# Performance work log

Measured on AMD Instinct MI355X. Metric: run time of the kernel, lower is better.

Reference implementation:

```python
import jax, jax.numpy as jnp
import numpy as np

S = 100000   # unique_source_num
T = 20000    # unique_target_num
N = S + T    # total nodes (sources first, then targets)
E = 1000000  # edges
SRC_DIM, EMB_DIM, TGT_DIM = 256, 128, 128


def setup_inputs() -> dict:
    key = jax.random.key(0)
    ks = jax.random.split(key, 6)
    source_feat = jax.random.normal(ks[0], (N, SRC_DIM), dtype=jnp.float32)
    src_idx = jax.random.randint(ks[1], (E,), 0, S)            # edge sources in [0, S)
    dst_idx = jax.random.randint(ks[2], (E,), 0, T)            # edge targets, target-local in [0, T)
    range_list = jax.random.randint(ks[3], (T, 2), 0, S)       # unused by the math (passed through in torch)
    # x_norm divides features; keep it bounded away from 0 like real row norms
    x_norm = jax.random.uniform(ks[4], (N,), dtype=jnp.float32, minval=0.5, maxval=1.5)
    k_e, k_w = jax.random.split(ks[5])
    embed = jax.random.normal(k_e, (SRC_DIM, EMB_DIM), dtype=jnp.float32)          # Param, std=1 init
    weight = jax.random.normal(k_w, (EMB_DIM, TGT_DIM), dtype=jnp.float32) / np.sqrt(EMB_DIM)  # is_after_relu std=1/sqrt(in)
    return {"source_feat": source_feat, "src_idx": src_idx, "dst_idx": dst_idx,
            "range_list": range_list, "x_norm": x_norm, "embed": embed, "weight": weight}


def reference(source_feat, src_idx, dst_idx, range_list, x_norm, embed, weight):
    # x = (source_feat @ embed) / x_norm[:, None]   -> [N, EMB_DIM]
    x = jnp.matmul(source_feat, embed) / x_norm[:, None]
    # message + scatter-mean aggregation onto targets (sources receive no edges,
    # so aggregating directly over the T targets == aggr_out[S:] in the torch code)
    msgs = x[src_idx]                                           # [E, EMB_DIM] gather
    summed = jax.ops.segment_sum(msgs, dst_idx, num_segments=T) # [T, EMB_DIM]
    cnt = jax.ops.segment_sum(jnp.ones((E,), dtype=x.dtype), dst_idx, num_segments=T)
    aggr = summed / jnp.maximum(cnt, 1.0)[:, None]              # mean; zero-degree -> 0
    out = jnp.matmul(aggr, weight)                              # [T, TGT_DIM]
    return out
```

## Files before the change

### kernel.cpp

```cpp
#include <hip/hip_runtime.h>
#include <cstdint>
#include <cstddef>

#define S_NUM 100000
#define T_NUM 20000
#define E_NUM 1000000

#define NB   1250
#define GT   16
#define CAP  1280
#define CH   4096
#define KB2  245
#define KB1  1563

typedef __bf16 bf16x8 __attribute__((ext_vector_type(8)));
typedef float f32x4 __attribute__((ext_vector_type(4)));

__device__ __forceinline__ unsigned short f2bf(float f) {
  unsigned int u = __float_as_uint(f);
  u += 0x7fffu + ((u >> 16) & 1u);
  return (unsigned short)(u >> 16);
}
__device__ __forceinline__ unsigned int f2bf2(float lo, float hi) {
  return (unsigned int)f2bf(lo) | ((unsigned int)f2bf(hi) << 16);
}
__device__ __forceinline__ float bflo(unsigned int v) { return __uint_as_float(v << 16); }
__device__ __forceinline__ float bfhi(unsigned int v) { return __uint_as_float(v & 0xffff0000u); }

__launch_bounds__(256)
__global__ void k0_prep(const float* __restrict__ embed, const float* __restrict__ weight,
                        int* __restrict__ gcursor, unsigned short* __restrict__ embedT,
                        unsigned short* __restrict__ weightT) {
  const int idx = blockIdx.x * 256 + threadIdx.x;
  if (idx < 2048) gcursor[idx] = 0;
  {
    const int col = idx & 127;
    const int k = idx >> 7;
    embedT[(size_t)col * 256 + k] = f2bf(embed[(size_t)k * 128 + col]);
  }
  if (idx < 16384) {
    const int n = idx & 127;
    const int k = idx >> 7;
    weightT[(size_t)n * 128 + k] = f2bf(weight[(size_t)k * 128 + n]);
  }
}

__launch_bounds__(512)
__global__ void k12_fused(const float* __restrict__ sf, const float* __restrict__ xn,
                          const unsigned short* __restrict__ embedT, unsigned short* __restrict__ xb,
                          const int* __restrict__ src_idx, const int* __restrict__ dst_idx,
                          int* __restrict__ gcursor, unsigned int* __restrict__ ebuf) {
  __shared__ __align__(16) unsigned char smem[64 * 296 * 2];
  const int tid = threadIdx.x;

  if (blockIdx.x < KB2) {
    int* bcnt  = (int*)smem;
    int* gbase = (int*)(smem + 5120);
    const int e0 = blockIdx.x * CH;
    const int e1 = (e0 + CH < E_NUM) ? (e0 + CH) : E_NUM;
    for (int i = tid; i < NB; i += 512) bcnt[i] = 0;
    __syncthreads();
    for (int e = e0 + tid; e < e1; e += 512)
      atomicAdd(&bcnt[dst_idx[e] >> 4], 1);
    __syncthreads();
    for (int i = tid; i < NB; i += 512) {
      const int cnt = bcnt[i];
      gbase[i] = (cnt > 0) ? atomicAdd(&gcursor[i], cnt) : 0;
      bcnt[i] = 0;
    }
    __syncthreads();
    for (int e = e0 + tid; e < e1; e += 512) {
      const int d = dst_idx[e];
      const int s = src_idx[e];
      const int b = d >> 4;
      const int r = atomicAdd(&bcnt[b], 1);
      const int pos = gbase[b] + r;
      if (pos < CAP)
        ebuf[(size_t)b * CAP + pos] = ((unsigned int)(d & 15) << 17) | (unsigned int)s;
    }
    return;
  }

  unsigned short (*lA)[296] = (unsigned short (*)[296])smem;
  unsigned short (*lC)[136] = (unsigned short (*)[136])smem;
  const int wave = tid >> 6;
  const int lane = tid & 63;
  const int quad = lane >> 4;
  const int l15 = lane & 15;
  const int row0 = (blockIdx.x - KB2) * 64;
  const int col0 = wave * 16;

  const unsigned short* ebT = embedT + (size_t)(col0 + l15) * 256;
  bf16x8 fb[8];
#pragma unroll
  for (int kc = 0; kc < 8; ++kc)
    fb[kc] = *(const bf16x8*)(ebT + kc * 32 + quad * 8);

#pragma unroll
  for (int i = 0; i < 4; ++i) {
    const int idx = i * 512 + tid;
    const int row = idx >> 5;
    const int seg = idx & 31;
    const float4* g = (const float4*)(sf + (size_t)(row0 + row) * 256 + seg * 8);
    const float4 v0 = g[0];
    const float4 v1 = g[1];
    uint4 pk;
    pk.x = f2bf2(v0.x, v0.y);
    pk.y = f2bf2(v0.z, v0.w);
    pk.z = f2bf2(v1.x, v1.y);
    pk.w = f2bf2(v1.z, v1.w);
    *(uint4*)&lA[row][seg * 8] = pk;
  }
  __syncthreads();

  f32x4 acc[4];
#pragma unroll
  for (int i = 0; i < 4; ++i) acc[i] = (f32x4){0.f, 0.f, 0.f, 0.f};

#pragma unroll
  for (int kc = 0; kc < 8; ++kc)
#pragma unroll
    for (int rt = 0; rt < 4; ++rt) {
      bf16x8 fa = *(const bf16x8*)&lA[rt * 16 + l15][kc * 32 + quad * 8];
      acc[rt] = __builtin_amdgcn_mfma_f32_16x16x32_bf16(fa, fb[kc], acc[rt], 0, 0, 0);
    }
  __syncthreads();

#pragma unroll
  for (int rt = 0; rt < 4; ++rt) {
#pragma unroll
    for (int reg = 0; reg < 4; ++reg) {
      const int row = rt * 16 + quad * 4 + reg;
      const float inv = __builtin_amdgcn_rcpf(xn[row0 + row]);
      lC[row][col0 + l15] = f2bf(acc[rt][reg] * inv);
    }
  }
  __syncthreads();

#pragma unroll
  for (int p = 0; p < 2; ++p) {
    const int i = p * 512 + tid;
    const int row = i >> 4;
    const int seg = i & 15;
    const int gr = row0 + row;
    if (gr < S_NUM)
      *(uint4*)(xb + (size_t)gr * 128 + seg * 8) = *(const uint4*)&lC[row][seg * 8];
  }
}

__launch_bounds__(512)
__global__ void k3_fused(const int* __restrict__ gcursor, const unsigned int* __restrict__ ebuf,
                         const unsigned short* __restrict__ xb,
                         const unsigned short* __restrict__ weightT,
                         float* __restrict__ out) {
  __shared__ unsigned int sls[CAP];
  __shared__ int hist[GT], scn[GT], cur[GT];
  __shared__ unsigned int Pu[GT][68];
  const int b = blockIdx.x;
  const int tid = threadIdx.x;
  const int wave = tid >> 6, lane = tid & 63;
  const int quad = lane >> 4, l15 = lane & 15;

  int n = gcursor[b];
  if (n > CAP) n = CAP;
  const unsigned int* eb = ebuf + (size_t)b * CAP;

  if (tid < GT) hist[tid] = 0;
  __syncthreads();
  for (int i = tid; i < n; i += 512) atomicAdd(&hist[eb[i] >> 17], 1);
  __syncthreads();
  if (tid == 0) {
    int run = 0;
#pragma unroll
    for (int i = 0; i < GT; ++i) { scn[i] = run; run += hist[i]; }
  }
  __syncthreads();
  if (tid < GT) cur[tid] = scn[tid];
  __syncthreads();
  for (int i = tid; i < n; i += 512) {
    const unsigned int e = eb[i];
    const int r = atomicAdd(&cur[e >> 17], 1);
    sls[r] = e & 0x1FFFFu;
  }
  __syncthreads();

  const int h = lane >> 5;
  const int cq = lane & 31;
#pragma unroll
  for (int rep = 0; rep < 2; ++rep) {
    const int tl = wave * 2 + rep;
    const int beg = scn[tl];
    const int c = hist[tl];
    float t0 = 0.f, t1 = 0.f, t2 = 0.f, t3 = 0.f;
    int e = 0;
    for (; e + 16 <= c; e += 16) {
      int s[8];
#pragma unroll
      for (int j = 0; j < 8; ++j) s[j] = (int)sls[beg + e + 2 * j + h];
      uint2 v[8];
#pragma unroll
      for (int j = 0; j < 8; ++j)
        v[j] = *(const uint2*)(xb + (size_t)s[j] * 128 + 4 * cq);
#pragma unroll
      for (int j = 0; j < 8; ++j) {
        t0 += bflo(v[j].x); t1 += bfhi(v[j].x);
        t2 += bflo(v[j].y); t3 += bfhi(v[j].y);
      }
    }
    for (; e + 2 <= c; e += 2) {
      const int s0 = (int)sls[beg + e + h];
      const uint2 v0 = *(const uint2*)(xb + (size_t)s0 * 128 + 4 * cq);
      t0 += bflo(v0.x); t1 += bfhi(v0.x);
      t2 += bflo(v0.y); t3 += bfhi(v0.y);
    }
    if ((c & 1) && h == 0) {
      const int s0 = (int)sls[beg + c - 1];
      const uint2 v0 = *(const uint2*)(xb + (size_t)s0 * 128 + 4 * cq);
      t0 += bflo(v0.x); t1 += bfhi(v0.x);
      t2 += bflo(v0.y); t3 += bfhi(v0.y);
    }
    t0 += __shfl_xor(t0, 32, 64);
    t1 += __shfl_xor(t1, 32, 64);
    t2 += __shfl_xor(t2, 32, 64);
    t3 += __shfl_xor(t3, 32, 64);
    const float inv = (c > 0) ? __builtin_amdgcn_rcpf((float)c) : 0.f;
    const unsigned int pk = h ? f2bf2(t2 * inv, t3 * inv) : f2bf2(t0 * inv, t1 * inv);
    Pu[tl][2 * cq + h] = pk;
  }
  __syncthreads();

  const int ncol = wave * 16 + l15;
  const unsigned short* wT = weightT + (size_t)ncol * 128;
  bf16x8 wb[4];
#pragma unroll
  for (int kc = 0; kc < 4; ++kc)
    wb[kc] = *(const bf16x8*)(wT + kc * 32 + quad * 8);
  f32x4 o0 = (f32x4){0.f, 0.f, 0.f, 0.f};
#pragma unroll
  for (int kc = 0; kc < 4; ++kc) {
    bf16x8 p0 = *(const bf16x8*)((const unsigned short*)&Pu[l15][0] + kc * 32 + quad * 8);
    o0 = __builtin_amdgcn_mfma_f32_16x16x32_bf16(p0, wb[kc], o0, 0, 0, 0);
  }
#pragma unroll
  for (int reg = 0; reg < 4; ++reg)
    out[((size_t)b * GT + quad * 4 + reg) * 128 + ncol] = o0[reg];
}

extern "C" void kernel_launch(void* const* d_in, const int* in_sizes, int n_in,
                              void* d_out, int out_size, void* d_ws, size_t ws_size,
                              hipStream_t stream) {
  const float* sf      = (const float*)d_in[0];
  const int*   src_idx = (const int*)d_in[1];
  const int*   dst_idx = (const int*)d_in[2];
  const float* xn      = (const float*)d_in[4];
  const float* embed   = (const float*)d_in[5];
  const float* weight  = (const float*)d_in[6];
  float* out = (float*)d_out;

  char* w = (char*)d_ws;
  unsigned short* xb      = (unsigned short*)(w);
  int* gcursor            = (int*)(w + 25600000);
  unsigned int* ebuf      = (unsigned int*)(w + 25608192);
  unsigned short* embedT  = (unsigned short*)(w + 32008192);
  unsigned short* weightT = (unsigned short*)(w + 32073728);

  k0_prep<<<128, 256, 0, stream>>>(embed, weight, gcursor, embedT, weightT);
  k12_fused<<<KB2 + KB1, 512, 0, stream>>>(sf, xn, embedT, xb, src_idx, dst_idx, gcursor, ebuf);
  k3_fused<<<NB, 512, 0, stream>>>(gcursor, ebuf, xb, weightT, out);
}
```

Baseline: 247.1 us.

## Merge all stages into one persistent kernel with atomic task queue

Replaces the three kernel launches with a single persistent kernel of NB blocks. Each block pulls tasks (prep, bucketing, GEMM tiles) from a global atomic counter, then runs the aggregation phase after spin-waiting on completion counters. A memset zeroes the control and cursor words, and the embed B-fragment loads are software-pipelined one k-chunk ahead. The goal is to remove launch gaps and tail effects between stages, at the cost of spin-waits that depend on all blocks being co-resident, plus serialised prep work.

```diff
diff --git a/kernel.cpp b/kernel.cpp
--- a/kernel.cpp
+++ b/kernel.cpp
@@ -12,6 +12,7 @@
 #define CH   4096
 #define KB2  245
 #define KB1  1563
+#define NTASK (1 + KB2 + KB1)
 
 typedef __bf16 bf16x8 __attribute__((ext_vector_type(8)));
 typedef float f32x4 __attribute__((ext_vector_type(4)));
@@ -27,139 +28,157 @@
 __device__ __forceinline__ float bflo(unsigned int v) { return __uint_as_float(v << 16); }
 __device__ __forceinline__ float bfhi(unsigned int v) { return __uint_as_float(v & 0xffff0000u); }
 
-__launch_bounds__(256)
-__global__ void k0_prep(const float* __restrict__ embed, const float* __restrict__ weight,
-                        int* __restrict__ gcursor, unsigned short* __restrict__ embedT,
-                        unsigned short* __restrict__ weightT) {
-  const int idx = blockIdx.x * 256 + threadIdx.x;
-  if (idx < 2048) gcursor[idx] = 0;
-  {
-    const int col = idx & 127;
-    const int k = idx >> 7;
-    embedT[(size_t)col * 256 + k] = f2bf(embed[(size_t)k * 128 + col]);
-  }
-  if (idx < 16384) {
-    const int n = idx & 127;
-    const int k = idx >> 7;
-    weightT[(size_t)n * 128 + k] = f2bf(weight[(size_t)k * 128 + n]);
-  }
-}
-
-__launch_bounds__(512)
-__global__ void k12_fused(const float* __restrict__ sf, const float* __restrict__ xn,
-                          const unsigned short* __restrict__ embedT, unsigned short* __restrict__ xb,
-                          const int* __restrict__ src_idx, const int* __restrict__ dst_idx,
-                          int* __restrict__ gcursor, unsigned int* __restrict__ ebuf) {
+__launch_bounds__(512, 4)
+__global__ void mega(const float* __restrict__ sf, const float* __restrict__ xn,
+                     const float* __restrict__ embed, const float* __restrict__ weight,
+                     const int* __restrict__ src_idx, const int* __restrict__ dst_idx,
+                     int* __restrict__ ctrl, int* __restrict__ gcursor,
+                     unsigned int* __restrict__ ebuf,
+                     unsigned short* __restrict__ embedT, unsigned short* __restrict__ weightT,
+                     unsigned short* __restrict__ xb, float* __restrict__ out) {
   __shared__ __align__(16) unsigned char smem[64 * 296 * 2];
-  const int tid = threadIdx.x;
-
-  if (blockIdx.x < KB2) {
-    int* bcnt  = (int*)smem;
-    int* gbase = (int*)(smem + 5120);
-    const int e0 = blockIdx.x * CH;
-    const int e1 = (e0 + CH < E_NUM) ? (e0 + CH) : E_NUM;
-    for (int i = tid; i < NB; i += 512) bcnt[i] = 0;
-    __syncthreads();
-    for (int e = e0 + tid; e < e1; e += 512)
-      atomicAdd(&bcnt[dst_idx[e] >> 4], 1);
-    __syncthreads();
-    for (int i = tid; i < NB; i += 512) {
-      const int cnt = bcnt[i];
-      gbase[i] = (cnt > 0) ? atomicAdd(&gcursor[i], cnt) : 0;
-      bcnt[i] = 0;
-    }
-    __syncthreads();
-    for (int e = e0 + tid; e < e1; e += 512) {
-      const int d = dst_idx[e];
-      const int s = src_idx[e];
-      const int b = d >> 4;
-      const int r = atomicAdd(&bcnt[b], 1);
-      const int pos = gbase[b] + r;
-      if (pos < CAP)
-        ebuf[(size_t)b * CAP + pos] = ((unsigned int)(d & 15) << 17) | (unsigned int)s;
-    }
-    return;
-  }
-
-  unsigned short (*lA)[296] = (unsigned short (*)[296])smem;
-  unsigned short (*lC)[136] = (unsigned short (*)[136])smem;
-  const int wave = tid >> 6;
-  const int lane = tid & 63;
-  const int quad = lane >> 4;
-  const int l15 = lane & 15;
-  const int row0 = (blockIdx.x - KB2) * 64;
-  const int col0 = wave * 16;
-
-  const unsigned short* ebT = embedT + (size_t)(col0 + l15) * 256;
-  bf16x8 fb[8];
-#pragma unroll
-  for (int kc = 0; kc < 8; ++kc)
-    fb[kc] = *(const bf16x8*)(ebT + kc * 32 + quad * 8);
-
-#pragma unroll
-  for (int i = 0; i < 4; ++i) {
-    const int idx = i * 512 + tid;
-    const int row = idx >> 5;
-    const int seg = idx & 31;
-    const float4* g = (const float4*)(sf + (size_t)(row0 + row) * 256 + seg * 8);
-    const float4 v0 = g[0];
-    const float4 v1 = g[1];
-    uint4 pk;
-    pk.x = f2bf2(v0.x, v0.y);
-    pk.y = f2bf2(v0.z, v0.w);
-    pk.z = f2bf2(v1.x, v1.y);
-    pk.w = f2bf2(v1.z, v1.w);
-    *(uint4*)&lA[row][seg * 8] = pk;
-  }
-  __syncthreads();
-
-  f32x4 acc[4];
-#pragma unroll
-  for (int i = 0; i < 4; ++i) acc[i] = (f32x4){0.f, 0.f, 0.f, 0.f};
-
-#pragma unroll
-  for (int kc = 0; kc < 8; ++kc)
-#pragma unroll
-    for (int rt = 0; rt < 4; ++rt) {
-      bf16x8 fa = *(const bf16x8*)&lA[rt * 16 + l15][kc * 32 + quad * 8];
-      acc[rt] = __builtin_amdgcn_mfma_f32_16x16x32_bf16(fa, fb[kc], acc[rt], 0, 0, 0);
-    }
-  __syncthreads();
-
-#pragma unroll
-  for (int rt = 0; rt < 4; ++rt) {
-#pragma unroll
-    for (int reg = 0; reg < 4; ++reg) {
-      const int row = rt * 16 + quad * 4 + reg;
-      const float inv = __builtin_amdgcn_rcpf(xn[row0 + row]);
-      lC[row][col0 + l15] = f2bf(acc[rt][reg] * inv);
-    }
-  }
-  __syncthreads();
-
-#pragma unroll
-  for (int p = 0; p < 2; ++p) {
-    const int i = p * 512 + tid;
-    const int row = i >> 4;
-    const int seg = i & 15;
-    const int gr = row0 + row;
-    if (gr < S_NUM)
-      *(uint4*)(xb + (size_t)gr * 128 + seg * 8) = *(const uint4*)&lC[row][seg * 8];
-  }
-}
-
-__launch_bounds__(512)
-__global__ void k3_fused(const int* __restrict__ gcursor, const unsigned int* __restrict__ ebuf,
-                         const unsigned short* __restrict__ xb,
-                         const unsigned short* __restrict__ weightT,
-                         float* __restrict__ out) {
-  __shared__ unsigned int sls[CAP];
-  __shared__ int hist[GT], scn[GT], cur[GT];
-  __shared__ unsigned int Pu[GT][68];
-  const int b = blockIdx.x;
+  __shared__ int stask;
   const int tid = threadIdx.x;
   const int wave = tid >> 6, lane = tid & 63;
   const int quad = lane >> 4, l15 = lane & 15;
+
+  int myTiles = 0;
+  bool embedReady = false;
+
+  for (;;) {
+    if (tid == 0) stask = atomicAdd(&ctrl[0], 1);
+    __syncthreads();
+    const int task = stask;
+    __syncthreads();
+    if (task >= NTASK) break;
+
+    if (task == 0) {
+      for (int i = tid; i < 32768; i += 512) {
+        const int col = i >> 8, k = i & 255;
+        embedT[col * 256 + k] = f2bf(embed[(size_t)k * 128 + col]);
+      }
+      for (int i = tid; i < 16384; i += 512) {
+        const int nn = i >> 7, k = i & 127;
+        weightT[nn * 128 + k] = f2bf(weight[(size_t)k * 128 + nn]);
+      }
+      __syncthreads();
+      if (tid == 0) { __threadfence(); atomicAdd(&ctrl[1], 1); }
+    } else if (task <= KB2) {
+      int* bcnt  = (int*)smem;
+      int* gbase = (int*)(smem + 5120);
+      const int e0 = (task - 1) * CH;
+      const int e1 = (e0 + CH < E_NUM) ? (e0 + CH) : E_NUM;
+      for (int i = tid; i < NB; i += 512) bcnt[i] = 0;
+      __syncthreads();
+      for (int e = e0 + tid; e < e1; e += 512)
+        atomicAdd(&bcnt[dst_idx[e] >> 4], 1);
+      __syncthreads();
+      for (int i = tid; i < NB; i += 512) {
+        const int cnt = bcnt[i];
+        gbase[i] = (cnt > 0) ? atomicAdd(&gcursor[i], cnt) : 0;
+        bcnt[i] = 0;
+      }
+      __syncthreads();
+      for (int e = e0 + tid; e < e1; e += 512) {
+        const int d = dst_idx[e];
+        const int s = src_idx[e];
+        const int bb = d >> 4;
+        const int r = atomicAdd(&bcnt[bb], 1);
+        const int pos = gbase[bb] + r;
+        if (pos < CAP)
+          ebuf[(size_t)bb * CAP + pos] = ((unsigned int)(d & 15) << 17) | (unsigned int)s;
+      }
+      __syncthreads();
+      if (tid == 0) { __threadfence(); atomicAdd(&ctrl[2], 1); }
+    } else {
+      if (!embedReady) {
+        if (tid == 0) {
+          while (__hip_atomic_load(&ctrl[1], __ATOMIC_ACQUIRE, __HIP_MEMORY_SCOPE_AGENT) == 0)
+            __builtin_amdgcn_s_sleep(2);
+          __threadfence();
+        }
+        __syncthreads();
+        embedReady = true;
+      }
+      unsigned short (*lA)[296] = (unsigned short (*)[296])smem;
+      unsigned short (*lC)[136] = (unsigned short (*)[136])smem;
+      const int row0 = (task - 1 - KB2) * 64;
+      const int col0 = wave * 16;
+      const unsigned short* ebT = embedT + (size_t)(col0 + l15) * 256;
+
+#pragma unroll
+      for (int i = 0; i < 4; ++i) {
+        const int idx = i * 512 + tid;
+        const int row = idx >> 5;
+        const int seg = idx & 31;
+        const float4* g = (const float4*)(sf + (size_t)(row0 + row) * 256 + seg * 8);
+        const float4 v0 = g[0];
+        const float4 v1 = g[1];
+        uint4 pk;
+        pk.x = f2bf2(v0.x, v0.y);
+        pk.y = f2bf2(v0.z, v0.w);
+        pk.z = f2bf2(v1.x, v1.y);
+        pk.w = f2bf2(v1.z, v1.w);
+        *(uint4*)&lA[row][seg * 8] = pk;
+      }
+      bf16x8 fbn = *(const bf16x8*)(ebT + quad * 8);
+      __syncthreads();
+
+      f32x4 acc[4];
+#pragma unroll
+      for (int i = 0; i < 4; ++i) acc[i] = (f32x4){0.f, 0.f, 0.f, 0.f};
+#pragma unroll
+      for (int kc = 0; kc < 8; ++kc) {
+        const bf16x8 fbc = fbn;
+        if (kc < 7) fbn = *(const bf16x8*)(ebT + (kc + 1) * 32 + quad * 8);
+#pragma unroll
+        for (int rt = 0; rt < 4; ++rt) {
+          bf16x8 fa = *(const bf16x8*)&lA[rt * 16 + l15][kc * 32 + quad * 8];
+          acc[rt] = __builtin_amdgcn_mfma_f32_16x16x32_bf16(fa, fbc, acc[rt], 0, 0, 0);
+        }
+      }
+      __syncthreads();
+
+#pragma unroll
+      for (int rt = 0; rt < 4; ++rt) {
+#pragma unroll
+        for (int reg = 0; reg < 4; ++reg) {
+          const int row = rt * 16 + quad * 4 + reg;
+          const float inv = __builtin_amdgcn_rcpf(xn[row0 + row]);
+          lC[row][col0 + l15] = f2bf(acc[rt][reg] * inv);
+        }
+      }
+      __syncthreads();
+
+#pragma unroll
+      for (int p = 0; p < 2; ++p) {
+        const int i = p * 512 + tid;
+        const int row = i >> 4;
+        const int seg = i & 15;
+        const int gr = row0 + row;
+        if (gr < S_NUM)
+          *(uint4*)(xb + (size_t)gr * 128 + seg * 8) = *(const uint4*)&lC[row][seg * 8];
+      }
+      ++myTiles;
+    }
+  }
+
+  if (tid == 0 && myTiles) { __threadfence(); atomicAdd(&ctrl[3], myTiles); }
+
+  const int b = blockIdx.x;
+
+  unsigned int* sls = (unsigned int*)smem;
+  int* hist = (int*)(smem + 5120);
+  int* scn  = (int*)(smem + 5184);
+  int* cur  = (int*)(smem + 5248);
+  unsigned int (*Pu)[68] = (unsigned int (*)[68])(smem + 5312);
+
+  if (tid == 0) {
+    while (__hip_atomic_load(&ctrl[2], __ATOMIC_ACQUIRE, __HIP_MEMORY_SCOPE_AGENT) < KB2)
+      __builtin_amdgcn_s_sleep(8);
+    __threadfence();
+  }
+  __syncthreads();
 
   int n = gcursor[b];
   if (n > CAP) n = CAP;
@@ -181,6 +200,14 @@
     const unsigned int e = eb[i];
     const int r = atomicAdd(&cur[e >> 17], 1);
     sls[r] = e & 0x1FFFFu;
+  }
+  __syncthreads();
+
+  if (tid == 0) {
+    while (__hip_atomic_load(&ctrl[3], __ATOMIC_ACQUIRE, __HIP_MEMORY_SCOPE_AGENT) < KB1 ||
+           __hip_atomic_load(&ctrl[1], __ATOMIC_ACQUIRE, __HIP_MEMORY_SCOPE_AGENT) == 0)
+      __builtin_amdgcn_s_sleep(8);
+    __threadfence();
   }
   __syncthreads();
 
@@ -259,12 +286,13 @@
 
   char* w = (char*)d_ws;
   unsigned short* xb      = (unsigned short*)(w);
-  int* gcursor            = (int*)(w + 25600000);
-  unsigned int* ebuf      = (unsigned int*)(w + 25608192);
-  unsigned short* embedT  = (unsigned short*)(w + 32008192);
-  unsigned short* weightT = (unsigned short*)(w + 32073728);
-
-  k0_prep<<<128, 256, 0, stream>>>(embed, weight, gcursor, embedT, weightT);
-  k12_fused<<<KB2 + KB1, 512, 0, stream>>>(sf, xn, embedT, xb, src_idx, dst_idx, gcursor, ebuf);
-  k3_fused<<<NB, 512, 0, stream>>>(gcursor, ebuf, xb, weightT, out);
-}
+  int* ctrl               = (int*)(w + 25600000);
+  int* gcursor            = (int*)(w + 25600064);
+  unsigned int* ebuf      = (unsigned int*)(w + 25608256);
+  unsigned short* embedT  = (unsigned short*)(w + 32008256);
+  unsigned short* weightT = (unsigned short*)(w + 32073792);
+
+  hipMemsetAsync(ctrl, 0, 8256, stream);
+  mega<<<NB, 512, 0, stream>>>(sf, xn, embed, weight, src_idx, dst_idx,
+                               ctrl, gcursor, ebuf, embedT, weightT, xb, out);
+}
```

Measured after the change: 698.2 us. 183% more time.

## Precompose embed@weight and aggregate raw bf16 source rows before one GEMM

Applied to the files above, without the earlier changes.

The matrices embed and weight are multiplied once in the prep kernel into a 256x128 composite. The per-node embedding GEMM over all 100k sources is dropped. Sources are instead stored as bf16 rows of length 256 already divided by x_norm, and the mean is taken over those 256-wide rows. Each target group then runs a single 256-deep MFMA with the composite, which removes the large GEMM but doubles the gathered bytes per edge and the size of the intermediate written to memory. The gather loop also now uses a full wave per row with software-prefetched indices.

```diff
diff --git a/kernel.cpp b/kernel.cpp
--- a/kernel.cpp
+++ b/kernel.cpp
@@ -11,7 +11,7 @@
 #define CAP  1280
 #define CH   4096
 #define KB2  245
-#define KB1  1563
+#define SB   1024
 
 typedef __bf16 bf16x8 __attribute__((ext_vector_type(8)));
 typedef float f32x4 __attribute__((ext_vector_type(4)));
@@ -29,33 +29,36 @@
 
 __launch_bounds__(256)
 __global__ void k0_prep(const float* __restrict__ embed, const float* __restrict__ weight,
-                        int* __restrict__ gcursor, unsigned short* __restrict__ embedT,
-                        unsigned short* __restrict__ weightT) {
-  const int idx = blockIdx.x * 256 + threadIdx.x;
-  if (idx < 2048) gcursor[idx] = 0;
-  {
-    const int col = idx & 127;
-    const int k = idx >> 7;
-    embedT[(size_t)col * 256 + k] = f2bf(embed[(size_t)k * 128 + col]);
-  }
-  if (idx < 16384) {
-    const int n = idx & 127;
-    const int k = idx >> 7;
-    weightT[(size_t)n * 128 + k] = f2bf(weight[(size_t)k * 128 + n]);
-  }
+                        int* __restrict__ gcursor, unsigned short* __restrict__ ewT) {
+  __shared__ float W[128][128];
+  const int tid = threadIdx.x;
+  const int b = blockIdx.x;
+  for (int i = tid; i < 16384; i += 256)
+    ((float*)W)[i] = weight[i];
+  const int gidx = b * 256 + tid;
+  if (gidx < 2048) gcursor[gidx] = 0;
+  __syncthreads();
+  const int r = tid >> 7;
+  const int n = tid & 127;
+  const int k = b * 2 + r;
+  float acc = 0.f;
+#pragma unroll 8
+  for (int j = 0; j < 128; ++j)
+    acc = fmaf(embed[(size_t)k * 128 + j], W[j][n], acc);
+  ewT[(size_t)n * 256 + k] = f2bf(acc);
 }
 
 __launch_bounds__(512)
 __global__ void k12_fused(const float* __restrict__ sf, const float* __restrict__ xn,
-                          const unsigned short* __restrict__ embedT, unsigned short* __restrict__ xb,
+                          unsigned short* __restrict__ sfb,
                           const int* __restrict__ src_idx, const int* __restrict__ dst_idx,
                           int* __restrict__ gcursor, unsigned int* __restrict__ ebuf) {
-  __shared__ __align__(16) unsigned char smem[64 * 296 * 2];
+  __shared__ int part[2560];
   const int tid = threadIdx.x;
 
   if (blockIdx.x < KB2) {
-    int* bcnt  = (int*)smem;
-    int* gbase = (int*)(smem + 5120);
+    int* bcnt  = part;
+    int* gbase = part + 1280;
     const int e0 = blockIdx.x * CH;
     const int e1 = (e0 + CH < E_NUM) ? (e0 + CH) : E_NUM;
     for (int i = tid; i < NB; i += 512) bcnt[i] = 0;
@@ -81,81 +84,31 @@
     return;
   }
 
-  unsigned short (*lA)[296] = (unsigned short (*)[296])smem;
-  unsigned short (*lC)[136] = (unsigned short (*)[136])smem;
-  const int wave = tid >> 6;
-  const int lane = tid & 63;
-  const int quad = lane >> 4;
-  const int l15 = lane & 15;
-  const int row0 = (blockIdx.x - KB2) * 64;
-  const int col0 = wave * 16;
-
-  const unsigned short* ebT = embedT + (size_t)(col0 + l15) * 256;
-  bf16x8 fb[8];
-#pragma unroll
-  for (int kc = 0; kc < 8; ++kc)
-    fb[kc] = *(const bf16x8*)(ebT + kc * 32 + quad * 8);
-
-#pragma unroll
-  for (int i = 0; i < 4; ++i) {
-    const int idx = i * 512 + tid;
-    const int row = idx >> 5;
-    const int seg = idx & 31;
-    const float4* g = (const float4*)(sf + (size_t)(row0 + row) * 256 + seg * 8);
+  const int bid = blockIdx.x - KB2;
+  for (int chunk = bid; chunk < 6250; chunk += SB) {
+    const int row = chunk * 16 + (tid >> 5);
+    const int seg = tid & 31;
+    const float4* g = (const float4*)(sf + (size_t)row * 256 + seg * 8);
     const float4 v0 = g[0];
     const float4 v1 = g[1];
+    const float inv = __builtin_amdgcn_rcpf(xn[row]);
     uint4 pk;
-    pk.x = f2bf2(v0.x, v0.y);
-    pk.y = f2bf2(v0.z, v0.w);
-    pk.z = f2bf2(v1.x, v1.y);
-    pk.w = f2bf2(v1.z, v1.w);
-    *(uint4*)&lA[row][seg * 8] = pk;
-  }
-  __syncthreads();
-
-  f32x4 acc[4];
-#pragma unroll
-  for (int i = 0; i < 4; ++i) acc[i] = (f32x4){0.f, 0.f, 0.f, 0.f};
-
-#pragma unroll
-  for (int kc = 0; kc < 8; ++kc)
-#pragma unroll
-    for (int rt = 0; rt < 4; ++rt) {
-      bf16x8 fa = *(const bf16x8*)&lA[rt * 16 + l15][kc * 32 + quad * 8];
-      acc[rt] = __builtin_amdgcn_mfma_f32_16x16x32_bf16(fa, fb[kc], acc[rt], 0, 0, 0);
-    }
-  __syncthreads();
-
-#pragma unroll
-  for (int rt = 0; rt < 4; ++rt) {
-#pragma unroll
-    for (int reg = 0; reg < 4; ++reg) {
-      const int row = rt * 16 + quad * 4 + reg;
-      const float inv = __builtin_amdgcn_rcpf(xn[row0 + row]);
-      lC[row][col0 + l15] = f2bf(acc[rt][reg] * inv);
-    }
-  }
-  __syncthreads();
-
-#pragma unroll
-  for (int p = 0; p < 2; ++p) {
-    const int i = p * 512 + tid;
-    const int row = i >> 4;
-    const int seg = i & 15;
-    const int gr = row0 + row;
-    if (gr < S_NUM)
-      *(uint4*)(xb + (size_t)gr * 128 + seg * 8) = *(const uint4*)&lC[row][seg * 8];
+    pk.x = f2bf2(v0.x * inv, v0.y * inv);
+    pk.y = f2bf2(v0.z * inv, v0.w * inv);
+    pk.z = f2bf2(v1.x * inv, v1.y * inv);
+    pk.w = f2bf2(v1.z * inv, v1.w * inv);
+    *(uint4*)(sfb + (size_t)row * 256 + seg * 8) = pk;
   }
 }
 
 __launch_bounds__(512)
 __global__ void k3_fused(const int* __restrict__ gcursor, const unsigned int* __restrict__ ebuf,
-                         const unsigned short* __restrict__ xb,
-                         const unsigned short* __restrict__ weightT,
+                         const unsigned short* __restrict__ sfb,
+                         const unsigned short* __restrict__ ewT,
                          float* __restrict__ out) {
   __shared__ unsigned int sls[CAP];
   __shared__ int hist[GT], scn[GT], cur[GT];
-  __shared__ unsigned int Pu[GT][68];
+  __shared__ unsigned int Pu[GT][132];
   const int b = blockIdx.x;
   const int tid = threadIdx.x;
   const int wave = tid >> 6, lane = tid & 63;
@@ -184,8 +137,6 @@
   }
   __syncthreads();
 
-  const int h = lane >> 5;
-  const int cq = lane & 31;
 #pragma unroll
   for (int rep = 0; rep < 2; ++rep) {
     const int tl = wave * 2 + rep;
@@ -193,51 +144,61 @@
     const int c = hist[tl];
     float t0 = 0.f, t1 = 0.f, t2 = 0.f, t3 = 0.f;
     int e = 0;
-    for (; e + 16 <= c; e += 16) {
-      int s[8];
-#pragma unroll
-      for (int j = 0; j < 8; ++j) s[j] = (int)sls[beg + e + 2 * j + h];
-      uint2 v[8];
-#pragma unroll
-      for (int j = 0; j < 8; ++j)
-        v[j] = *(const uint2*)(xb + (size_t)s[j] * 128 + 4 * cq);
-#pragma unroll
-      for (int j = 0; j < 8; ++j) {
-        t0 += bflo(v[j].x); t1 += bfhi(v[j].x);
-        t2 += bflo(v[j].y); t3 += bfhi(v[j].y);
+    if (c >= 8) {
+      int scur[8];
+#pragma unroll
+      for (int j = 0; j < 8; ++j) scur[j] = (int)sls[beg + j];
+      for (; e + 16 <= c; e += 8) {
+        uint2 v[8];
+#pragma unroll
+        for (int j = 0; j < 8; ++j)
+          v[j] = *(const uint2*)(sfb + (size_t)scur[j] * 256 + 4 * lane);
+        int snext[8];
+#pragma unroll
+        for (int j = 0; j < 8; ++j)
+          snext[j] = (int)sls[beg + e + 8 + j];
+#pragma unroll
+        for (int j = 0; j < 8; ++j) {
+          t0 += bflo(v[j].x); t1 += bfhi(v[j].x);
+          t2 += bflo(v[j].y); t3 += bfhi(v[j].y);
+        }
+#pragma unroll
+        for (int j = 0; j < 8; ++j) scur[j] = snext[j];
       }
-    }
-    for (; e + 2 <= c; e += 2) {
-      const int s0 = (int)sls[beg + e + h];
-      const uint2 v0 = *(const uint2*)(xb + (size_t)s0 * 128 + 4 * cq);
+      {
+        uint2 v[8];
+#pragma unroll
+        for (int j = 0; j < 8; ++j)
+          v[j] = *(const uint2*)(sfb + (size_t)scur[j] * 256 + 4 * lane);
+#pragma unroll
+        for (int j = 0; j < 8; ++j) {
+          t0 += bflo(v[j].x); t1 += bfhi(v[j].x);
+          t2 += bflo(v[j].y); t3 += bfhi(v[j].y);
+        }
+        e += 8;
+      }
+    }
+    for (; e < c; ++e) {
+      const int s0 = (int)sls[beg + e];
+      const uint2 v0 = *(const uint2*)(sfb + (size_t)s0 * 256 + 4 * lane);
       t0 += bflo(v0.x); t1 += bfhi(v0.x);
       t2 += bflo(v0.y); t3 += bfhi(v0.y);
     }
-    if ((c & 1) && h == 0) {
-      const int s0 = (int)sls[beg + c - 1];
-      const uint2 v0 = *(const uint2*)(xb + (size_t)s0 * 128 + 4 * cq);
-      t0 += bflo(v0.x); t1 += bfhi(v0.x);
-      t2 += bflo(v0.y); t3 += bfhi(v0.y);
-    }
-    t0 += __shfl_xor(t0, 32, 64);
-    t1 += __shfl_xor(t1, 32, 64);
-    t2 += __shfl_xor(t2, 32, 64);
-    t3 += __shfl_xor(t3, 32, 64);
     const float inv = (c > 0) ? __builtin_amdgcn_rcpf((float)c) : 0.f;
-    const unsigned int pk = h ? f2bf2(t2 * inv, t3 * inv) : f2bf2(t0 * inv, t1 * inv);
-    Pu[tl][2 * cq + h] = pk;
+    Pu[tl][2 * lane]     = f2bf2(t0 * inv, t1 * inv);
+    Pu[tl][2 * lane + 1] = f2bf2(t2 * inv, t3 * inv);
   }
   __syncthreads();
 
   const int ncol = wave * 16 + l15;
-  const unsigned short* wT = weightT + (size_t)ncol * 128;
-  bf16x8 wb[4];
-#pragma unroll
-  for (int kc = 0; kc < 4; ++kc)
+  const unsigned short* wT = ewT + (size_t)ncol * 256;
+  bf16x8 wb[8];
+#pragma unroll
+  for (int kc = 0; kc < 8; ++kc)
     wb[kc] = *(const bf16x8*)(wT + kc * 32 + quad * 8);
   f32x4 o0 = (f32x4){0.f, 0.f, 0.f, 0.f};
 #pragma unroll
-  for (int kc = 0; kc < 4; ++kc) {
+  for (int kc = 0; kc < 8; ++kc) {
     bf16x8 p0 = *(const bf16x8*)((const unsigned short*)&Pu[l15][0] + kc * 32 + quad * 8);
     o0 = __builtin_amdgcn_mfma_f32_16x16x32_bf16(p0, wb[kc], o0, 0, 0, 0);
   }
@@ -258,13 +219,12 @@
   float* out = (float*)d_out;
 
   char* w = (char*)d_ws;
-  unsigned short* xb      = (unsigned short*)(w);
-  int* gcursor            = (int*)(w + 25600000);
-  unsigned int* ebuf      = (unsigned int*)(w + 25608192);
-  unsigned short* embedT  = (unsigned short*)(w + 32008192);
-  unsigned short* weightT = (unsigned short*)(w + 32073728);
-
-  k0_prep<<<128, 256, 0, stream>>>(embed, weight, gcursor, embedT, weightT);
-  k12_fused<<<KB2 + KB1, 512, 0, stream>>>(sf, xn, embedT, xb, src_idx, dst_idx, gcursor, ebuf);
-  k3_fused<<<NB, 512, 0, stream>>>(gcursor, ebuf, xb, weightT, out);
-}
+  unsigned short* sfb = (unsigned short*)(w);
+  int* gcursor        = (int*)(w + 51200000);
+  unsigned int* ebuf  = (unsigned int*)(w + 51208192);
+  unsigned short* ewT = (unsigned short*)(w + 57608192);
+
+  k0_prep<<<128, 256, 0, stream>>>(embed, weight, gcursor, ewT);
+  k12_fused<<<KB2 + SB, 512, 0, stream>>>(sf, xn, sfb, src_idx, dst_idx, gcursor, ebuf);
+  k3_fused<<<NB, 512, 0, stream>>>(gcursor, ebuf, sfb, ewT, out);
+}
```

After: 284.7 us. 15.2% more time.

## Stage source features via direct global-to-LDS loads and reorder fused block roles

Applied to the files above, without the earlier changes.

The GEMM blocks now bring the fp32 source-feature tile into LDS with global_load_lds 16-byte transfers, bypassing registers. They then read it back, convert it to bf16 and store it into the padded layout that feeds the MFMA loop. The block order is swapped so GEMM blocks come first and edge-binning blocks run last, and launch bounds request 4 blocks per CU. LDS grows to 64KB per block and a round trip through LDS is added, which may limit occupancy and adds extra LDS traffic and barriers.

```diff
diff --git a/kernel.cpp b/kernel.cpp
--- a/kernel.cpp
+++ b/kernel.cpp
@@ -15,6 +15,8 @@
 
 typedef __bf16 bf16x8 __attribute__((ext_vector_type(8)));
 typedef float f32x4 __attribute__((ext_vector_type(4)));
+typedef unsigned int u32_g __attribute__((address_space(1)));
+typedef unsigned int u32_l __attribute__((address_space(3)));
 
 __device__ __forceinline__ unsigned short f2bf(float f) {
   unsigned int u = __float_as_uint(f);
@@ -45,18 +47,18 @@
   }
 }
 
-__launch_bounds__(512)
+__launch_bounds__(512, 4)
 __global__ void k12_fused(const float* __restrict__ sf, const float* __restrict__ xn,
                           const unsigned short* __restrict__ embedT, unsigned short* __restrict__ xb,
                           const int* __restrict__ src_idx, const int* __restrict__ dst_idx,
                           int* __restrict__ gcursor, unsigned int* __restrict__ ebuf) {
-  __shared__ __align__(16) unsigned char smem[64 * 296 * 2];
+  __shared__ __align__(16) unsigned char smem[65536];
   const int tid = threadIdx.x;
 
-  if (blockIdx.x < KB2) {
+  if (blockIdx.x >= KB1) {
     int* bcnt  = (int*)smem;
     int* gbase = (int*)(smem + 5120);
-    const int e0 = blockIdx.x * CH;
+    const int e0 = (blockIdx.x - KB1) * CH;
     const int e1 = (e0 + CH < E_NUM) ? (e0 + CH) : E_NUM;
     for (int i = tid; i < NB; i += 512) bcnt[i] = 0;
     __syncthreads();
@@ -81,42 +83,50 @@
     return;
   }
 
-  unsigned short (*lA)[296] = (unsigned short (*)[296])smem;
-  unsigned short (*lC)[136] = (unsigned short (*)[136])smem;
   const int wave = tid >> 6;
   const int lane = tid & 63;
   const int quad = lane >> 4;
   const int l15 = lane & 15;
-  const int row0 = (blockIdx.x - KB2) * 64;
+  const int row0 = blockIdx.x * 64;
   const int col0 = wave * 16;
-
   const unsigned short* ebT = embedT + (size_t)(col0 + l15) * 256;
+
+  {
+    const char* gsrc = (const char*)(sf + (size_t)row0 * 256);
+#pragma unroll
+    for (int j = 0; j < 8; ++j) {
+      const char* gp = gsrc + (size_t)(j * 512 + tid) * 16;
+      unsigned char* lp = smem + (size_t)(j * 512 + wave * 64) * 16;
+      __builtin_amdgcn_global_load_lds((const u32_g*)gp, (u32_l*)lp, 16, 0, 0);
+    }
+  }
   bf16x8 fb[8];
 #pragma unroll
   for (int kc = 0; kc < 8; ++kc)
     fb[kc] = *(const bf16x8*)(ebT + kc * 32 + quad * 8);
-
-#pragma unroll
-  for (int i = 0; i < 4; ++i) {
-    const int idx = i * 512 + tid;
-    const int row = idx >> 5;
-    const int seg = idx & 31;
-    const float4* g = (const float4*)(sf + (size_t)(row0 + row) * 256 + seg * 8);
-    const float4 v0 = g[0];
-    const float4 v1 = g[1];
-    uint4 pk;
-    pk.x = f2bf2(v0.x, v0.y);
-    pk.y = f2bf2(v0.z, v0.w);
-    pk.z = f2bf2(v1.x, v1.y);
-    pk.w = f2bf2(v1.z, v1.w);
-    *(uint4*)&lA[row][seg * 8] = pk;
+  __syncthreads();
+
+  f32x4 vf[8];
+#pragma unroll
+  for (int k = 0; k < 8; ++k)
+    vf[k] = *(const f32x4*)(smem + (size_t)tid * 16 + (size_t)k * 8192);
+  __syncthreads();
+  unsigned short (*lA)[296] = (unsigned short (*)[296])smem;
+  unsigned short (*lC)[136] = (unsigned short (*)[136])smem;
+#pragma unroll
+  for (int k = 0; k < 8; ++k) {
+    const int r = wave + 8 * k;
+    const int c = lane * 4;
+    uint2 pk;
+    pk.x = f2bf2(vf[k][0], vf[k][1]);
+    pk.y = f2bf2(vf[k][2], vf[k][3]);
+    *(uint2*)&lA[r][c] = pk;
   }
   __syncthreads();
 
   f32x4 acc[4];
 #pragma unroll
   for (int i = 0; i < 4; ++i) acc[i] = (f32x4){0.f, 0.f, 0.f, 0.f};
-
 #pragma unroll
   for (int kc = 0; kc < 8; ++kc)
 #pragma unroll
@@ -265,6 +275,6 @@
   unsigned short* weightT = (unsigned short*)(w + 32073728);
 
   k0_prep<<<128, 256, 0, stream>>>(embed, weight, gcursor, embedT, weightT);
-  k12_fused<<<KB2 + KB1, 512, 0, stream>>>(sf, xn, embedT, xb, src_idx, dst_idx, gcursor, ebuf);
+  k12_fused<<<KB1 + KB2, 512, 0, stream>>>(sf, xn, embedT, xb, src_idx, dst_idx, gcursor, ebuf);
   k3_fused<<<NB, 512, 0, stream>>>(gcursor, ebuf, xb, weightT, out);
 }
```

Measured after the change: 255.7 us. 1.03x slower.
